# Performance work log

Measured on AMD Instinct MI355X. Metric: run time of the kernel, lower is better.

## Reference

```python
import jax, jax.numpy as jnp
import numpy as np

N = 100000
E = 600000
IN_DIM = 256
H0 = 128
H1 = 64
EPS = 1e-5


def setup_inputs() -> dict:
    key = jax.random.key(0)
    ks = jax.random.split(key, 12)
    x = jax.random.normal(ks[0], (N, IN_DIM), dtype=jnp.float32)
    edge_index = jax.random.randint(ks[1], (2, E), 0, N, dtype=jnp.int64)
    edge_weight = jax.random.uniform(ks[2], (E,), dtype=jnp.float32)
    def lin(k, fan_in, fan_out):
        bound = 1.0 / np.sqrt(fan_in)
        k1, k2 = jax.random.split(k)
        W = jax.random.uniform(k1, (fan_in, fan_out), minval=-bound, maxval=bound, dtype=jnp.float32)
        b = jax.random.uniform(k2, (fan_out,), minval=-bound, maxval=bound, dtype=jnp.float32)
        return W, b
    W0, b0 = lin(ks[3], IN_DIM, H0)
    W1, b1 = lin(ks[4], H0, H0)
    W2, b2 = lin(ks[5], H0, H0)
    pW, pb = lin(ks[6], H0, H1)
    return {
        'x': x, 'edge_index': edge_index, 'edge_weight': edge_weight,
        'bn_gamma': jnp.ones((IN_DIM,), jnp.float32), 'bn_beta': jnp.zeros((IN_DIM,), jnp.float32),
        'W0': W0, 'b0': b0, 'W1': W1, 'b1': b1, 'W2': W2, 'b2': b2,
        'pbn_gamma': jnp.ones((H0,), jnp.float32), 'pbn_beta': jnp.zeros((H0,), jnp.float32),
        'pW': pW, 'pb': pb,
    }


def batchnorm(x, gamma, beta):
    # BatchNorm1d training-mode forward: per-feature batch statistics over nodes
    mean = jnp.mean(x, axis=0)
    var = jnp.mean(jnp.square(x - mean), axis=0)  # biased var, as torch BN forward
    return (x - mean) * jax.lax.rsqrt(var + EPS) * gamma + beta


def gcn_conv(x, src, dst, norm, W, b):
    # PyG GCNConv (add_self_loops=False): transform then normalized aggregation
    h = x @ W                                   # [N, out]
    msg = norm[:, None] * h[src]                # gather + scale, [E, out]
    out = jax.ops.segment_sum(msg, dst, num_segments=N)  # scatter-add
    return out + b


def reference(x, edge_index, edge_weight, bn_gamma, bn_beta, W0, b0, W1, b1, W2, b2, pbn_gamma, pbn_beta, pW, pb):
    src, dst = edge_index[0], edge_index[1]
    # gcn_norm without self loops: D^-1/2 A D^-1/2
    deg = jax.ops.segment_sum(edge_weight, dst, num_segments=N)
    dis = jnp.where(deg > 0, jax.lax.rsqrt(jnp.maximum(deg, EPS)), 0.0)
    norm = dis[src] * edge_weight * dis[dst]    # [E]

    h = batchnorm(x, bn_gamma, bn_beta)
    h = jax.nn.relu(gcn_conv(h, src, dst, norm, W0, b0))
    h = jax.nn.relu(gcn_conv(h, src, dst, norm, W1, b1))
    h = jax.nn.relu(gcn_conv(h, src, dst, norm, W2, b2))
    # project head: BN -> Linear -> ReLU
    h = batchnorm(h, pbn_gamma, pbn_beta)
    h = jax.nn.relu(h @ pW + pb)
    return h
```

## Files before the change

kernel.cpp:

```cpp
#include <hip/hip_runtime.h>


constexpr int NN    = 100000;
constexpr int NEDGE = 600000;
constexpr int INDIM = 256;
constexpr int HD    = 128;
constexpr int OUTD  = 64;
constexpr int EB    = (NEDGE + 255) / 256;
constexpr int SB    = 1024;
constexpr int NB    = (NN + 255) / 256;
constexpr int WB    = 257;
constexpr int GG    = (NN + 127) / 128;
constexpr int A2B   = 1024;
#define EPSV 1e-5f

typedef __bf16 bf16x8 __attribute__((ext_vector_type(8)));
typedef float  f32x4  __attribute__((ext_vector_type(4)));

__device__ __forceinline__ float bf2f(unsigned short u) {
    unsigned int v = ((unsigned int)u) << 16;
    return __builtin_bit_cast(float, v);
}
__device__ __forceinline__ unsigned short f2bf(float f) {
    __bf16 h = (__bf16)f;
    return __builtin_bit_cast(unsigned short, h);
}
__device__ __forceinline__ void atomAdd(float* p, float v) {
    unsafeAtomicAdd(p, v);
}

template <int K, int M, bool RELU_OUT, bool OUT_BF16>
__device__ __forceinline__ void mgemm_body(int bid, int tid, char* smem,
                                           const unsigned short* __restrict__ A,
                                           const unsigned short* __restrict__ Bt,
                                           const float* __restrict__ outBias,
                                           void* __restrict__ Craw, int n) {
    constexpr int BK  = 64;
    constexpr int LDA = BK + 8;
    unsigned short* As = (unsigned short*)smem;
    unsigned short* Bs = As + 128 * LDA;

    const int wave = tid >> 6, lane = tid & 63;
    const int quad = lane >> 4, mrow = lane & 15;
    const int row0 = bid * 128;

    constexpr int RT = (M == 128) ? 4 : 2;
    constexpr int CT = 4;
    const int rowbase = (M == 128) ? ((wave >> 1) * 64) : (wave * 32);
    const int colbase = (M == 128) ? ((wave & 1) * 64) : 0;

    f32x4 acc[RT][CT];
#pragma unroll
    for (int i = 0; i < RT; i++)
#pragma unroll
        for (int j = 0; j < CT; j++) acc[i][j] = (f32x4){0.f, 0.f, 0.f, 0.f};

    for (int k0 = 0; k0 < K; k0 += BK) {
        if (k0) __syncthreads();
#pragma unroll
        for (int p = 0; p < 4; p++) {
            int c   = p * 256 + tid;
            int r   = c >> 3;
            int c8  = (c & 7) * 8;
            int grow = row0 + r;
            uint4 u = make_uint4(0, 0, 0, 0);
            if (grow < n) u = *(const uint4*)&A[(size_t)grow * K + k0 + c8];
            *(uint4*)&As[r * LDA + c8] = u;
        }
#pragma unroll
        for (int p = 0; p < M / 32; p++) {
            int c  = p * 256 + tid;
            int r  = c >> 3;
            int c8 = (c & 7) * 8;
            *(uint4*)&Bs[r * LDA + c8] = *(const uint4*)&Bt[(size_t)r * K + k0 + c8];
        }
        __syncthreads();

#pragma unroll
        for (int ks = 0; ks < BK; ks += 32) {
            bf16x8 af[RT], bfr[CT];
#pragma unroll
            for (int i = 0; i < RT; i++)
                af[i] = *(const bf16x8*)&As[(rowbase + i * 16 + mrow) * LDA + ks + quad * 8];
#pragma unroll
            for (int j = 0; j < CT; j++)
                bfr[j] = *(const bf16x8*)&Bs[(colbase + j * 16 + mrow) * LDA + ks + quad * 8];
#pragma unroll
            for (int i = 0; i < RT; i++)
#pragma unroll
                for (int j = 0; j < CT; j++)
                    acc[i][j] = __builtin_amdgcn_mfma_f32_16x16x32_bf16(
                        af[i], bfr[j], acc[i][j], 0, 0, 0);
        }
    }

#pragma unroll
    for (int i = 0; i < RT; i++) {
#pragma unroll
        for (int r = 0; r < 4; r++) {
            int row = row0 + rowbase + i * 16 + quad * 4 + r;
            if (row < n) {
#pragma unroll
                for (int j = 0; j < CT; j++) {
                    int col = colbase + j * 16 + mrow;
                    float v = acc[i][j][r];
                    if (outBias) v += outBias[col];
                    if (RELU_OUT) v = fmaxf(v, 0.f);
                    if (OUT_BF16)
                        ((unsigned short*)Craw)[(size_t)row * M + col] = f2bf(v);
                    else
                        ((float*)Craw)[(size_t)row * M + col] = v;
                }
            }
        }
    }
}

template <bool L1>
__device__ __forceinline__ void gather8(const unsigned short* __restrict__ tg,
                                        uint2* __restrict__ edata,
                                        const float* __restrict__ dis,
                                        float id, int gl,
                                        int i, int beg, int end, float* acc) {
    uint4 v[8]; float w[8]; uint2 ed[8];
#pragma unroll
    for (int k = 0; k < 8; k++) {
        int  idx = i + k;
        bool ok  = idx < end;
        ed[k] = edata[ok ? idx : beg];
    }
#pragma unroll
    for (int k = 0; k < 8; k++) {
        bool ok = (i + k) < end;
        float wt = __builtin_bit_cast(float, ed[k].y);
        if (L1) wt = dis[ed[k].x] * wt * id;
        w[k] = ok ? wt : 0.f;
        v[k] = *(const uint4*)&tg[(size_t)ed[k].x * HD];
    }
    if (L1) {
#pragma unroll
        for (int k = 0; k < 8; k++)
            if (gl == 0 && (i + k) < end)
                edata[i + k].y = __builtin_bit_cast(unsigned, w[k]);
    }
#pragma unroll
    for (int k = 0; k < 8; k++) {
        acc[0] += w[k] * bf2f((unsigned short)(v[k].x & 0xffff));
        acc[1] += w[k] * bf2f((unsigned short)(v[k].x >> 16));
        acc[2] += w[k] * bf2f((unsigned short)(v[k].y & 0xffff));
        acc[3] += w[k] * bf2f((unsigned short)(v[k].y >> 16));
        acc[4] += w[k] * bf2f((unsigned short)(v[k].z & 0xffff));
        acc[5] += w[k] * bf2f((unsigned short)(v[k].z >> 16));
        acc[6] += w[k] * bf2f((unsigned short)(v[k].w & 0xffff));
        acc[7] += w[k] * bf2f((unsigned short)(v[k].w >> 16));
    }
}

template <bool L1>
__global__ __launch_bounds__(256) void fagg_gemm_k(const unsigned short* __restrict__ t,
                                                   const int* __restrict__ rowptr,
                                                   uint2* __restrict__ edata,
                                                   const float* __restrict__ dis,
                                                   const float* __restrict__ bias,
                                                   const unsigned short* __restrict__ Bt,
                                                   unsigned short* __restrict__ Cout,
                                                   int n) {
    constexpr int LDAa = HD + 8;
    constexpr int LDAb = 64 + 8;
    __shared__ unsigned short As[128 * LDAa];
    __shared__ unsigned short Bs[HD * LDAb];

    const int tid  = threadIdx.x;
    const int row0 = blockIdx.x * 128;

    {
        const int g  = tid >> 4;
        const int gl = tid & 15;
        const unsigned short* tg = t + gl * 8;
        float4 bb0 = *(const float4*)&bias[gl * 8];
        float4 bb1 = *(const float4*)&bias[gl * 8 + 4];
        for (int rr = 0; rr < 8; rr++) {
            int node = row0 + g * 8 + rr;
            float acc[8];
#pragma unroll
            for (int j = 0; j < 8; j++) acc[j] = 0.f;
            if (node < n) {
                int beg = rowptr[node], end = rowptr[node + 1];
                float id = L1 ? dis[node] : 0.f;
                for (int i = beg; i < end; i += 8)
                    gather8<L1>(tg, edata, dis, id, gl, i, beg, end, acc);
            }
            float r0 = fmaxf(acc[0] + bb0.x, 0.f), r1 = fmaxf(acc[1] + bb0.y, 0.f);
            float r2 = fmaxf(acc[2] + bb0.z, 0.f), r3 = fmaxf(acc[3] + bb0.w, 0.f);
            float r4 = fmaxf(acc[4] + bb1.x, 0.f), r5 = fmaxf(acc[5] + bb1.y, 0.f);
            float r6 = fmaxf(acc[6] + bb1.z, 0.f), r7 = fmaxf(acc[7] + bb1.w, 0.f);
            uint4 o;
            o.x = (unsigned int)f2bf(r0) | ((unsigned int)f2bf(r1) << 16);
            o.y = (unsigned int)f2bf(r2) | ((unsigned int)f2bf(r3) << 16);
            o.z = (unsigned int)f2bf(r4) | ((unsigned int)f2bf(r5) << 16);
            o.w = (unsigned int)f2bf(r6) | ((unsigned int)f2bf(r7) << 16);
            *(uint4*)&As[(g * 8 + rr) * LDAa + gl * 8] = o;
        }
    }

    const int wave = tid >> 6, lane = tid & 63;
    const int quad = lane >> 4, mrow = lane & 15;
    const int rowbase = (wave >> 1) * 64;
    const int colbase = (wave & 1) * 64;

    f32x4 acc[4][4];
#pragma unroll
    for (int i = 0; i < 4; i++)
#pragma unroll
        for (int j = 0; j < 4; j++) acc[i][j] = (f32x4){0.f, 0.f, 0.f, 0.f};

    for (int k0 = 0; k0 < HD; k0 += 64) {
        if (k0) __syncthreads();
#pragma unroll
        for (int p = 0; p < 4; p++) {
            int c  = p * 256 + tid;
            int r  = c >> 3;
            int c8 = (c & 7) * 8;
            *(uint4*)&Bs[r * LDAb + c8] = *(const uint4*)&Bt[(size_t)r * HD + k0 + c8];
        }
        __syncthreads();
#pragma unroll
        for (int ks = 0; ks < 64; ks += 32) {
            bf16x8 af[4], bfr[4];
#pragma unroll
            for (int i = 0; i < 4; i++)
                af[i] = *(const bf16x8*)&As[(rowbase + i * 16 + mrow) * LDAa + k0 + ks + quad * 8];
#pragma unroll
            for (int j = 0; j < 4; j++)
                bfr[j] = *(const bf16x8*)&Bs[(colbase + j * 16 + mrow) * LDAb + ks + quad * 8];
#pragma unroll
            for (int i = 0; i < 4; i++)
#pragma unroll
                for (int j = 0; j < 4; j++)
                    acc[i][j] = __builtin_amdgcn_mfma_f32_16x16x32_bf16(
                        af[i], bfr[j], acc[i][j], 0, 0, 0);
        }
    }

#pragma unroll
    for (int i = 0; i < 4; i++) {
#pragma unroll
        for (int r = 0; r < 4; r++) {
            int row = row0 + rowbase + i * 16 + quad * 4 + r;
            if (row < n) {
#pragma unroll
                for (int j = 0; j < 4; j++) {
                    int col = colbase + j * 16 + mrow;
                    Cout[(size_t)row * HD + col] = f2bf(acc[i][j][r]);
                }
            }
        }
    }
}

__global__ __launch_bounds__(256) void front_k(const int* __restrict__ dst,
                                               int* __restrict__ cnt,
                                               int* __restrict__ rank,
                                               const float* __restrict__ x,
                                               float* __restrict__ sums,
                                               unsigned short* __restrict__ xb) {
    __shared__ float red[256 * 8];
    const int tid = threadIdx.x;
    if (blockIdx.x < EB) {
        int i = blockIdx.x * 256 + tid;
        if (i < NEDGE) {
            int d = dst[i];
            rank[i] = atomicAdd(&cnt[d], 1);
        }
        return;
    }
    const int bid = blockIdx.x - EB;
    const int cg  = tid & 63;
    const int rs  = tid >> 6;
    float s0 = 0.f, s1 = 0.f, s2 = 0.f, s3 = 0.f;
    float q0 = 0.f, q1 = 0.f, q2 = 0.f, q3 = 0.f;
    for (int r0 = bid * 16; r0 < NN; r0 += SB * 16) {
        float4 v[4];
#pragma unroll
        for (int j = 0; j < 4; j++)
            v[j] = *(const float4*)&x[(size_t)(r0 + rs + j * 4) * INDIM + cg * 4];
#pragma unroll
        for (int j = 0; j < 4; j++) {
            s0 += v[j].x; s1 += v[j].y; s2 += v[j].z; s3 += v[j].w;
            q0 += v[j].x * v[j].x; q1 += v[j].y * v[j].y;
            q2 += v[j].z * v[j].z; q3 += v[j].w * v[j].w;
            unsigned int w0 = (unsigned int)f2bf(v[j].x) | ((unsigned int)f2bf(v[j].y) << 16);
            unsigned int w1 = (unsigned int)f2bf(v[j].z) | ((unsigned int)f2bf(v[j].w) << 16);
            *(uint2*)&xb[(size_t)(r0 + rs + j * 4) * INDIM + cg * 4] = make_uint2(w0, w1);
        }
    }
    red[tid * 8 + 0] = s0; red[tid * 8 + 1] = s1;
    red[tid * 8 + 2] = s2; red[tid * 8 + 3] = s3;
    red[tid * 8 + 4] = q0; red[tid * 8 + 5] = q1;
    red[tid * 8 + 6] = q2; red[tid * 8 + 7] = q3;
    __syncthreads();
    int cgr = tid >> 2, j = tid & 3;
    float a = 0.f, b = 0.f;
#pragma unroll
    for (int r2 = 0; r2 < 4; r2++) {
        a += red[(r2 * 64 + cgr) * 8 + j];
        b += red[(r2 * 64 + cgr) * 8 + 4 + j];
    }
    atomAdd(&sums[tid], a);
    atomAdd(&sums[INDIM + tid], b);
}

__global__ __launch_bounds__(256) void mid_k(const int* __restrict__ cnt,
                                             int* __restrict__ rowptr,
                                             int* __restrict__ bsum,
                                             const float* __restrict__ stats,
                                             const float* __restrict__ gamma,
                                             const float* __restrict__ beta,
                                             const float* __restrict__ W0,
                                             const float* __restrict__ W1,
                                             const float* __restrict__ W2,
                                             unsigned short* __restrict__ W0t,
                                             unsigned short* __restrict__ W1t,
                                             unsigned short* __restrict__ W2t,
                                             float* __restrict__ d0, float invN) {
    __shared__ float sm[512];
    const int tid = threadIdx.x;
    if (blockIdx.x < NB) {
        int* s = (int*)sm;
        int i = blockIdx.x * 256 + tid;
        s[tid] = (i < NN) ? cnt[i] : 0;
        __syncthreads();
        for (int d = 1; d < 256; d <<= 1) {
            int t = (tid >= d) ? s[tid - d] : 0;
            __syncthreads();
            s[tid] += t;
            __syncthreads();
        }
        if (i < NN) rowptr[i + 1] = s[tid];
        if (tid == 255) bsum[blockIdx.x] = s[255];
        return;
    }
    const int b = blockIdx.x - NB;
    float* sA = sm;
    float* sC = sm + 256;
    {
        float mean = stats[tid] * invN;
        float var  = stats[INDIM + tid] * invN - mean * mean;
        float a    = gamma[tid] * rsqrtf(var + EPSV);
        sA[tid] = a;
        sC[tid] = beta[tid] - mean * a;
    }
    __syncthreads();
    if (b < 128) {
        int i = b * 256 + tid, k = i >> 7, j = i & 127;
        W0t[(size_t)j * INDIM + k] = f2bf(W0[i] * sA[k]);
    } else if (b < 192) {
        int i = (b - 128) * 256 + tid, k = i >> 7, j = i & 127;
        W1t[(size_t)j * HD + k] = f2bf(W1[i]);
    } else if (b < 256) {
        int i = (b - 192) * 256 + tid, k = i >> 7, j = i & 127;
        W2t[(size_t)j * HD + k] = f2bf(W2[i]);
    } else {
        if (tid < HD) {
            float s = 0.f;
            for (int ff = 0; ff < INDIM; ff++) s += sC[ff] * W0[ff * HD + tid];
            d0[tid] = s;
        }
    }
}

__global__ __launch_bounds__(512) void scan2_k(int* __restrict__ bsum, int nb) {
    __shared__ int s[512];
    s[threadIdx.x] = (threadIdx.x < (unsigned)nb) ? bsum[threadIdx.x] : 0;
    __syncthreads();
    for (int d = 1; d < 512; d <<= 1) {
        int t = (threadIdx.x >= d) ? s[threadIdx.x - d] : 0;
        __syncthreads();
        s[threadIdx.x] += t;
        __syncthreads();
    }
    if (threadIdx.x < (unsigned)nb) bsum[threadIdx.x] = s[threadIdx.x];
}

__global__ __launch_bounds__(256) void scan3_k(int* __restrict__ rowptr,
                                               const int* __restrict__ bsum, int n) {
    int i = blockIdx.x * 256 + threadIdx.x;
    if (i == 0) rowptr[0] = 0;
    if (i < n) {
        int v = rowptr[i + 1];
        if (blockIdx.x > 0) v += bsum[blockIdx.x - 1];
        rowptr[i + 1] = v;
    }
}

__global__ __launch_bounds__(256) void sg0_k(const int* __restrict__ src,
                                             const int* __restrict__ dst,
                                             const float* __restrict__ ew,
                                             const int* __restrict__ rank,
                                             const int* __restrict__ rowptr,
                                             uint2* __restrict__ edata,
                                             const unsigned short* __restrict__ xb,
                                             const unsigned short* __restrict__ W0t,
                                             const float* __restrict__ d0,
                                             unsigned short* __restrict__ tbufA) {
    __shared__ char smem[(128 * 72 + 128 * 72) * 2];
    if (blockIdx.x < EB) {
        int i = blockIdx.x * 256 + threadIdx.x;
        if (i < NEDGE) {
            int s = src[i], d = dst[i];
            int p = rowptr[d] + rank[i];
            edata[p] = make_uint2((unsigned)s, __builtin_bit_cast(unsigned, ew[i]));
        }
        return;
    }
    mgemm_body<INDIM, HD, false, true>(blockIdx.x - EB, threadIdx.x, smem,
                                       xb, W0t, d0, tbufA, NN);
}

__global__ __launch_bounds__(256) void degnorm_k(const int* __restrict__ rowptr,
                                                 const uint2* __restrict__ edata,
                                                 float* __restrict__ dis) {
    int n = blockIdx.x * 256 + threadIdx.x;
    if (n < NN) {
        int beg = rowptr[n], end = rowptr[n + 1];
        float s = 0.f;
        for (int j = beg; j < end; j++)
            s += __builtin_bit_cast(float, edata[j].y);
        dis[n] = (s > 0.f) ? rsqrtf(fmaxf(s, EPSV)) : 0.f;
    }
}

__global__ __launch_bounds__(256) void agg2_stats_k(const unsigned short* __restrict__ t,
                                                    const int* __restrict__ rowptr,
                                                    uint2* __restrict__ edata,
                                                    const float* __restrict__ bias,
                                                    unsigned short* __restrict__ agg,
                                                    float* __restrict__ sums, int n) {
    const int tid = threadIdx.x, g = tid >> 4, gl = tid & 15;
    const unsigned short* tg = t + gl * 8;
    float4 bb0 = *(const float4*)&bias[gl * 8];
    float4 bb1 = *(const float4*)&bias[gl * 8 + 4];
    float ssum[8], ssq[8];
#pragma unroll
    for (int j = 0; j < 8; j++) { ssum[j] = 0.f; ssq[j] = 0.f; }

    for (int node0 = blockIdx.x * 16; node0 < n; node0 += A2B * 16) {
        int node = node0 + g;
        float acc[8];
#pragma unroll
        for (int j = 0; j < 8; j++) acc[j] = 0.f;
        if (node < n) {
            int beg = rowptr[node], end = rowptr[node + 1];
            for (int i = beg; i < end; i += 8)
                gather8<false>(tg, edata, nullptr, 0.f, gl, i, beg, end, acc);
        }
        float r[8];
        r[0] = fmaxf(acc[0] + bb0.x, 0.f); r[1] = fmaxf(acc[1] + bb0.y, 0.f);
        r[2] = fmaxf(acc[2] + bb0.z, 0.f); r[3] = fmaxf(acc[3] + bb0.w, 0.f);
        r[4] = fmaxf(acc[4] + bb1.x, 0.f); r[5] = fmaxf(acc[5] + bb1.y, 0.f);
        r[6] = fmaxf(acc[6] + bb1.z, 0.f); r[7] = fmaxf(acc[7] + bb1.w, 0.f);
        if (node < n) {
            uint4 o;
            o.x = (unsigned int)f2bf(r[0]) | ((unsigned int)f2bf(r[1]) << 16);
            o.y = (unsigned int)f2bf(r[2]) | ((unsigned int)f2bf(r[3]) << 16);
            o.z = (unsigned int)f2bf(r[4]) | ((unsigned int)f2bf(r[5]) << 16);
            o.w = (unsigned int)f2bf(r[6]) | ((unsigned int)f2bf(r[7]) << 16);
            *(uint4*)&agg[(size_t)node * HD + gl * 8] = o;
#pragma unroll
            for (int j = 0; j < 8; j++) { ssum[j] += r[j]; ssq[j] += r[j] * r[j]; }
        }
    }

    __shared__ float red[256 * 16];
#pragma unroll
    for (int j = 0; j < 8; j++) {
        red[tid * 16 + j]     = ssum[j];
        red[tid * 16 + 8 + j] = ssq[j];
    }
    __syncthreads();
    if (tid < HD) {
        int glr = tid >> 3, j = tid & 7;
        float a = 0.f, b = 0.f;
#pragma unroll
        for (int g2 = 0; g2 < 16; g2++) {
            a += red[(g2 * 16 + glr) * 16 + j];
            b += red[(g2 * 16 + glr) * 16 + 8 + j];
        }
        atomAdd(&sums[tid], a);
        atomAdd(&sums[HD + tid], b);
    }
}

__global__ __launch_bounds__(256) void wprep2_k(const float* __restrict__ stats2,
                                                const float* __restrict__ gamma,
                                                const float* __restrict__ beta,
                                                const float* __restrict__ pW,
                                                const float* __restrict__ pb,
                                                unsigned short* __restrict__ pWt,
                                                float* __restrict__ dfin, float invN) {
    __shared__ float sA[HD], sC[HD];
    int f = threadIdx.x;
    if (f < HD) {
        float mean = stats2[f] * invN;
        float var  = stats2[HD + f] * invN - mean * mean;
        float a    = gamma[f] * rsqrtf(var + EPSV);
        sA[f] = a;
        sC[f] = beta[f] - mean * a;
    }
    __syncthreads();
    int b = blockIdx.x, tid = threadIdx.x;
    if (b < 32) {
        int i = b * 256 + tid, k = i >> 6, j = i & 63;
        pWt[(size_t)j * HD + k] = f2bf(pW[i] * sA[k]);
    } else {
        if (tid < OUTD) {
            float s = pb[tid];
            for (int ff = 0; ff < HD; ff++) s += sC[ff] * pW[ff * OUTD + tid];
            dfin[tid] = s;
        }
    }
}

__global__ __launch_bounds__(256) void gemm3_k(const unsigned short* __restrict__ A,
                                               const unsigned short* __restrict__ Bt,
                                               const float* __restrict__ outBias,
                                               float* __restrict__ C, int n) {
    __shared__ char smem[(128 * 72 + OUTD * 72) * 2];
    mgemm_body<HD, OUTD, true, false>(blockIdx.x, threadIdx.x, smem,
                                      A, Bt, outBias, C, n);
}

extern "C" void kernel_launch(void* const* d_in, const int* in_sizes, int n_in,
                              void* d_out, int out_size, void* d_ws, size_t ws_size,
                              hipStream_t stream) {
    const float* x        = (const float*)d_in[0];
    const int*   ei       = (const int*)d_in[1];
    const float* ew       = (const float*)d_in[2];
    const float* bn_gamma = (const float*)d_in[3];
    const float* bn_beta  = (const float*)d_in[4];
    const float* W0       = (const float*)d_in[5];
    const float* b0       = (const float*)d_in[6];
    const float* W1       = (const float*)d_in[7];
    const float* b1       = (const float*)d_in[8];
    const float* W2       = (const float*)d_in[9];
    const float* b2       = (const float*)d_in[10];
    const float* pgamma   = (const float*)d_in[11];
    const float* pbeta    = (const float*)d_in[12];
    const float* pW       = (const float*)d_in[13];
    const float* pb       = (const float*)d_in[14];
    float* out = (float*)d_out;

    const int* srcp = ei;
    const int* dstp = ei + NEDGE;

    char*  base = (char*)d_ws;
    size_t off  = 0;
    auto carve = [&](size_t bytes) -> void* {
        void* p = (void*)(base + off);
        off = (off + bytes + 255) & ~(size_t)255;
        return p;
    };
    int*            cnt    = (int*)carve(NN * 4);
    float*          stats  = (float*)carve(2 * INDIM * 4);
    float*          stats2 = (float*)carve(2 * HD * 4);
    int*            rowptr = (int*)carve((NN + 1) * 4);
    int*            rank   = (int*)carve((size_t)NEDGE * 4);
    float*          dis    = (float*)carve(NN * 4);
    int*            bsum   = (int*)carve(512 * 4);
    uint2*          edata  = (uint2*)carve((size_t)NEDGE * 8);
    float*          d0     = (float*)carve(HD * 4);
    float*          dfin   = (float*)carve(OUTD * 4);
    unsigned short* W0t    = (unsigned short*)carve((size_t)INDIM * HD * 2);
    unsigned short* W1t    = (unsigned short*)carve((size_t)HD * HD * 2);
    unsigned short* W2t    = (unsigned short*)carve((size_t)HD * HD * 2);
    unsigned short* pWt    = (unsigned short*)carve((size_t)HD * OUTD * 2);
    unsigned short* xb     = (unsigned short*)carve((size_t)NN * INDIM * 2);
    unsigned short* tbufA  = (unsigned short*)carve((size_t)NN * HD * 2);
    unsigned short* tbufB  = (unsigned short*)carve((size_t)NN * HD * 2);
    unsigned short* aggb   = (unsigned short*)carve((size_t)NN * HD * 2);
    (void)ws_size;

    hipMemsetAsync(cnt, 0, (size_t)((char*)stats2 - (char*)cnt) + 2 * HD * 4, stream);

    front_k<<<EB + SB, 256, 0, stream>>>(dstp, cnt, rank, x, stats, xb);

    mid_k<<<NB + WB, 256, 0, stream>>>(cnt, rowptr, bsum, stats, bn_gamma, bn_beta,
                                       W0, W1, W2, W0t, W1t, W2t, d0, 1.f / NN);
    scan2_k<<<1, 512, 0, stream>>>(bsum, NB);
    scan3_k<<<NB, 256, 0, stream>>>(rowptr, bsum, NN);

    sg0_k<<<EB + GG, 256, 0, stream>>>(srcp, dstp, ew, rank, rowptr, edata,
                                       xb, W0t, d0, tbufA);

    degnorm_k<<<NB, 256, 0, stream>>>(rowptr, edata, dis);

    fagg_gemm_k<true><<<GG, 256, 0, stream>>>(tbufA, rowptr, edata, dis, b0, W1t, tbufB, NN);
    fagg_gemm_k<false><<<GG, 256, 0, stream>>>(tbufB, rowptr, edata, dis, b1, W2t, tbufA, NN);

    agg2_stats_k<<<A2B, 256, 0, stream>>>(tbufA, rowptr, edata, b2, aggb, stats2, NN);

    wprep2_k<<<33, 256, 0, stream>>>(stats2, pgamma, pbeta, pW, pb, pWt, dfin,
                                     1.f / NN);
    gemm3_k<<<GG, 256, 0, stream>>>(aggb, pWt, dfin, out, NN);

    (void)n_in; (void)in_sizes; (void)out_size;
}
```

Measured before the change: 455.3 us.

## Drop bf16 copy of x; convert fp32 input inside first GEMM load

The front kernel no longer writes a bf16 copy of x. The first GEMM now reads fp32 x directly and packs it to bf16 while staging tiles into shared memory. This removes a 51MB write and a 51MB read, at the cost of reading 102MB of fp32 during the GEMM instead of 51MB of bf16. The block layouts of front_k and sg0_k are also interleaved: edge-counting and stats blocks alternate, and scatter blocks are mixed 3:1 with GEMM blocks, so both kinds of work overlap on the GPU.

After: 523.8 us. 15.0% more time.

```diff
diff --git a/kernel.cpp b/kernel.cpp
--- a/kernel.cpp
+++ b/kernel.cpp
@@ -25,13 +25,16 @@
     __bf16 h = (__bf16)f;
     return __builtin_bit_cast(unsigned short, h);
 }
+__device__ __forceinline__ unsigned int pk2(float a, float b) {
+    return (unsigned int)f2bf(a) | ((unsigned int)f2bf(b) << 16);
+}
 __device__ __forceinline__ void atomAdd(float* p, float v) {
     unsafeAtomicAdd(p, v);
 }
 
-template <int K, int M, bool RELU_OUT, bool OUT_BF16>
+template <int K, int M, bool RELU_OUT, bool OUT_BF16, bool A_F32>
 __device__ __forceinline__ void mgemm_body(int bid, int tid, char* smem,
-                                           const unsigned short* __restrict__ A,
+                                           const void* __restrict__ Araw,
                                            const unsigned short* __restrict__ Bt,
                                            const float* __restrict__ outBias,
                                            void* __restrict__ Craw, int n) {
@@ -64,7 +67,18 @@
             int c8  = (c & 7) * 8;
             int grow = row0 + r;
             uint4 u = make_uint4(0, 0, 0, 0);
-            if (grow < n) u = *(const uint4*)&A[(size_t)grow * K + k0 + c8];
+            if (grow < n) {
+                if constexpr (A_F32) {
+                    const float* Af = (const float*)Araw;
+                    float4 fa = *(const float4*)&Af[(size_t)grow * K + k0 + c8];
+                    float4 fb = *(const float4*)&Af[(size_t)grow * K + k0 + c8 + 4];
+                    u.x = pk2(fa.x, fa.y); u.y = pk2(fa.z, fa.w);
+                    u.z = pk2(fb.x, fb.y); u.w = pk2(fb.z, fb.w);
+                } else {
+                    const unsigned short* Ab = (const unsigned short*)Araw;
+                    u = *(const uint4*)&Ab[(size_t)grow * K + k0 + c8];
+                }
+            }
             *(uint4*)&As[r * LDA + c8] = u;
         }
 #pragma unroll
@@ -195,10 +209,10 @@
             float r4 = fmaxf(acc[4] + bb1.x, 0.f), r5 = fmaxf(acc[5] + bb1.y, 0.f);
             float r6 = fmaxf(acc[6] + bb1.z, 0.f), r7 = fmaxf(acc[7] + bb1.w, 0.f);
             uint4 o;
-            o.x = (unsigned int)f2bf(r0) | ((unsigned int)f2bf(r1) << 16);
-            o.y = (unsigned int)f2bf(r2) | ((unsigned int)f2bf(r3) << 16);
-            o.z = (unsigned int)f2bf(r4) | ((unsigned int)f2bf(r5) << 16);
-            o.w = (unsigned int)f2bf(r6) | ((unsigned int)f2bf(r7) << 16);
+            o.x = pk2(r0, r1);
+            o.y = pk2(r2, r3);
+            o.z = pk2(r4, r5);
+            o.w = pk2(r6, r7);
             *(uint4*)&As[(g * 8 + rr) * LDAa + gl * 8] = o;
         }
     }
@@ -262,19 +276,18 @@
                                                int* __restrict__ cnt,
                                                int* __restrict__ rank,
                                                const float* __restrict__ x,
-                                               float* __restrict__ sums,
-                                               unsigned short* __restrict__ xb) {
+                                               float* __restrict__ sums) {
     __shared__ float red[256 * 8];
     const int tid = threadIdx.x;
-    if (blockIdx.x < EB) {
-        int i = blockIdx.x * 256 + tid;
-        if (i < NEDGE) {
+    const int bx  = blockIdx.x;
+    if ((bx & 1) == 0) {
+        for (int i = (bx >> 1) * 256 + tid; i < NEDGE; i += 1024 * 256) {
             int d = dst[i];
             rank[i] = atomicAdd(&cnt[d], 1);
         }
         return;
     }
-    const int bid = blockIdx.x - EB;
+    const int bid = bx >> 1;
     const int cg  = tid & 63;
     const int rs  = tid >> 6;
     float s0 = 0.f, s1 = 0.f, s2 = 0.f, s3 = 0.f;
@@ -289,9 +302,6 @@
             s0 += v[j].x; s1 += v[j].y; s2 += v[j].z; s3 += v[j].w;
             q0 += v[j].x * v[j].x; q1 += v[j].y * v[j].y;
             q2 += v[j].z * v[j].z; q3 += v[j].w * v[j].w;
-            unsigned int w0 = (unsigned int)f2bf(v[j].x) | ((unsigned int)f2bf(v[j].y) << 16);
-            unsigned int w1 = (unsigned int)f2bf(v[j].z) | ((unsigned int)f2bf(v[j].w) << 16);
-            *(uint2*)&xb[(size_t)(r0 + rs + j * 4) * INDIM + cg * 4] = make_uint2(w0, w1);
         }
     }
     red[tid * 8 + 0] = s0; red[tid * 8 + 1] = s1;
@@ -399,13 +409,15 @@
                                              const int* __restrict__ rank,
                                              const int* __restrict__ rowptr,
                                              uint2* __restrict__ edata,
-                                             const unsigned short* __restrict__ xb,
+                                             const float* __restrict__ x,
                                              const unsigned short* __restrict__ W0t,
                                              const float* __restrict__ d0,
                                              unsigned short* __restrict__ tbufA) {
     __shared__ char smem[(128 * 72 + 128 * 72) * 2];
-    if (blockIdx.x < EB) {
-        int i = blockIdx.x * 256 + threadIdx.x;
+    const int bx = blockIdx.x;
+    if ((bx & 3) != 3) {
+        int sid = 3 * (bx >> 2) + (bx & 3);
+        int i = sid * 256 + threadIdx.x;
         if (i < NEDGE) {
             int s = src[i], d = dst[i];
             int p = rowptr[d] + rank[i];
@@ -413,8 +425,8 @@
         }
         return;
     }
-    mgemm_body<INDIM, HD, false, true>(blockIdx.x - EB, threadIdx.x, smem,
-                                       xb, W0t, d0, tbufA, NN);
+    mgemm_body<INDIM, HD, false, true, true>(bx >> 2, threadIdx.x, smem,
+                                             x, W0t, d0, tbufA, NN);
 }
 
 __global__ __launch_bounds__(256) void degnorm_k(const int* __restrict__ rowptr,
@@ -461,10 +473,10 @@
         r[6] = fmaxf(acc[6] + bb1.z, 0.f); r[7] = fmaxf(acc[7] + bb1.w, 0.f);
         if (node < n) {
             uint4 o;
-            o.x = (unsigned int)f2bf(r[0]) | ((unsigned int)f2bf(r[1]) << 16);
-            o.y = (unsigned int)f2bf(r[2]) | ((unsigned int)f2bf(r[3]) << 16);
-            o.z = (unsigned int)f2bf(r[4]) | ((unsigned int)f2bf(r[5]) << 16);
-            o.w = (unsigned int)f2bf(r[6]) | ((unsigned int)f2bf(r[7]) << 16);
+            o.x = pk2(r[0], r[1]);
+            o.y = pk2(r[2], r[3]);
+            o.z = pk2(r[4], r[5]);
+            o.w = pk2(r[6], r[7]);
             *(uint4*)&agg[(size_t)node * HD + gl * 8] = o;
 #pragma unroll
             for (int j = 0; j < 8; j++) { ssum[j] += r[j]; ssq[j] += r[j] * r[j]; }
@@ -526,8 +538,8 @@
                                                const float* __restrict__ outBias,
                                                float* __restrict__ C, int n) {
     __shared__ char smem[(128 * 72 + OUTD * 72) * 2];
-    mgemm_body<HD, OUTD, true, false>(blockIdx.x, threadIdx.x, smem,
-                                      A, Bt, outBias, C, n);
+    mgemm_body<HD, OUTD, true, false, false>(blockIdx.x, threadIdx.x, smem,
+                                             A, Bt, outBias, C, n);
 }
 
 extern "C" void kernel_launch(void* const* d_in, const int* in_sizes, int n_in,
@@ -574,7 +586,6 @@
     unsigned short* W1t    = (unsigned short*)carve((size_t)HD * HD * 2);
     unsigned short* W2t    = (unsigned short*)carve((size_t)HD * HD * 2);
     unsigned short* pWt    = (unsigned short*)carve((size_t)HD * OUTD * 2);
-    unsigned short* xb     = (unsigned short*)carve((size_t)NN * INDIM * 2);
     unsigned short* tbufA  = (unsigned short*)carve((size_t)NN * HD * 2);
     unsigned short* tbufB  = (unsigned short*)carve((size_t)NN * HD * 2);
     unsigned short* aggb   = (unsigned short*)carve((size_t)NN * HD * 2);
@@ -582,15 +593,15 @@
 
     hipMemsetAsync(cnt, 0, (size_t)((char*)stats2 - (char*)cnt) + 2 * HD * 4, stream);
 
-    front_k<<<EB + SB, 256, 0, stream>>>(dstp, cnt, rank, x, stats, xb);
+    front_k<<<2048, 256, 0, stream>>>(dstp, cnt, rank, x, stats);
 
     mid_k<<<NB + WB, 256, 0, stream>>>(cnt, rowptr, bsum, stats, bn_gamma, bn_beta,
                                        W0, W1, W2, W0t, W1t, W2t, d0, 1.f / NN);
     scan2_k<<<1, 512, 0, stream>>>(bsum, NB);
     scan3_k<<<NB, 256, 0, stream>>>(rowptr, bsum, NN);
 
-    sg0_k<<<EB + GG, 256, 0, stream>>>(srcp, dstp, ew, rank, rowptr, edata,
-                                       xb, W0t, d0, tbufA);
+    sg0_k<<<GG * 4, 256, 0, stream>>>(srcp, dstp, ew, rank, rowptr, edata,
+                                      x, W0t, d0, tbufA);
 
     degnorm_k<<<NB, 256, 0, stream>>>(rowptr, edata, dis);
 
```
